# Kernel tuning notes

Measured on AMD Instinct MI355X. Metric: run time of the kernel, lower is better.

Reference implementation:

```python
import jax, jax.numpy as jnp
import numpy as np
from jax import lax

EPS = 1e-8

def int8_fq(x):
    # Int8ActPerTensorFloat: per-tensor float scale from runtime max-abs, fake-quant with STE.
    s = jnp.maximum(jnp.max(jnp.abs(x)) / 127.0, EPS)
    q = jnp.clip(jnp.round(x / s), -128.0, 127.0) * s
    return x + lax.stop_gradient(q - x)

def bin_w(w):
    # BINARY weight quant: per-tensor scale = mean(|w|), weights -> +/- scale (STE).
    s = jnp.mean(jnp.abs(w))
    wq = jnp.where(w >= 0, s, -s)
    return w + lax.stop_gradient(wq - w)

def qrelu(x):
    # QuantReLU with int8 input_quant and int8 act_quant
    return int8_fq(jax.nn.relu(int8_fq(x)))

def conv2d(x, w, b):
    y = lax.conv_general_dilated(x, w, window_strides=(1, 1), padding='VALID',
                                 dimension_numbers=('NCHW', 'OIHW', 'NCHW'))
    return y + b[None, :, None, None]

def maxpool2(x):
    return lax.reduce_window(x, -jnp.inf, lax.max, (1, 1, 2, 2), (1, 1, 2, 2), 'VALID')

def setup_inputs() -> dict:
    key = jax.random.key(0)
    ks = jax.random.split(key, 12)
    B = 16384
    inp = {
        'input_tensor': jax.random.normal(ks[0], (B, 3, 32, 32), dtype=jnp.float32),
        'w1': jax.random.normal(ks[1], (6, 3, 5, 5), dtype=jnp.float32) * 0.1,
        'b1': jax.random.normal(ks[2], (6,), dtype=jnp.float32) * 0.01,
        'w2': jax.random.normal(ks[3], (16, 6, 5, 5), dtype=jnp.float32) * 0.1,
        'b2': jax.random.normal(ks[4], (16,), dtype=jnp.float32) * 0.01,
        'fw1': jax.random.normal(ks[5], (120, 400), dtype=jnp.float32) * 0.05,
        'fb1': jax.random.normal(ks[6], (120,), dtype=jnp.float32) * 0.01,
        'fw2': jax.random.normal(ks[7], (84, 120), dtype=jnp.float32) * 0.05,
        'fb2': jax.random.normal(ks[8], (84,), dtype=jnp.float32) * 0.01,
        'fw3': jax.random.normal(ks[9], (10, 84), dtype=jnp.float32) * 0.05,
        'fb3': jax.random.normal(ks[10], (10,), dtype=jnp.float32) * 0.01,
    }
    return inp

def reference(input_tensor, w1, b1, w2, b2, fw1, fb1, fw2, fb2, fw3, fb3):
    x = int8_fq(input_tensor)                  # QuantIdentity
    x = qrelu(conv2d(x, bin_w(w1), b1))        # conv1 + relu1: [B,6,28,28]
    x = maxpool2(x)                            # [B,6,14,14]
    x = qrelu(conv2d(x, bin_w(w2), b2))        # conv2 + relu2: [B,16,10,10]
    x = maxpool2(x)                            # [B,16,5,5]
    x = x.reshape(x.shape[0], -1)              # [B,400]
    x = qrelu(x @ bin_w(fw1).T + fb1)          # fc1 + relu3: [B,120]
    x = qrelu(x @ bin_w(fw2).T + fb2)          # fc2 + relu4: [B,84]
    out = x @ bin_w(fw3).T + fb3               # fc3: [B,10]
    return out
```

## Files before the change

### kernel.cpp

```cpp
#include <hip/hip_runtime.h>
#include <math.h>

#define BATCH 16384
#define EPSQ 1e-8f

#define OFF_SCAL 0
#define OFF_WPK1 16
#define OFF_WPK2 196
#define OFF_FQ1  1156
#define OFF_FQ2  13156
#define OFF_FQ3  15844
#define OFF_A    16384
#define OFF_QIN   OFF_A
#define OFF_QC2   OFF_A
#define OFF_ISUM2 (OFF_A + 6000000)
#define OFF_QC3   (OFF_A + 10000000)
#define OFF_P3    (OFF_A + 12000000)
#define OFF_P4    (OFF_A + 14000000)
#define OFF_ISUM1 (OFF_A + 18874368)

__device__ inline int sdot4(unsigned int a, unsigned int b, int c) {
    return __builtin_amdgcn_sdot4((int)a, (int)b, c, false);
}

__device__ inline unsigned int fkey(float f) {
    unsigned int u = __float_as_uint(f);
    return (u & 0x80000000u) ? ~u : (u | 0x80000000u);
}
__device__ inline float fdec(unsigned int k) {
    unsigned int u = (k & 0x80000000u) ? (k ^ 0x80000000u) : ~k;
    return __uint_as_float(u);
}
#define KEY_ZERO   0x80000000u
#define KEY_NEGINF 0x007FFFFFu

__device__ inline float waveMax(float v) {
    #pragma unroll
    for (int off = 32; off > 0; off >>= 1)
        v = fmaxf(v, __shfl_down(v, off, 64));
    return v;
}

__device__ inline void blockAtomicMax2(float vmax, float vnmax,
                                       unsigned int* gmax, unsigned int* gnmax) {
    __shared__ float sm[4], sn[4];
    float a = waveMax(vmax), b = waveMax(vnmax);
    int tid = threadIdx.x;
    if ((tid & 63) == 0) { sm[tid >> 6] = a; sn[tid >> 6] = b; }
    __syncthreads();
    if (tid == 0) {
        atomicMax(gmax, fkey(fmaxf(fmaxf(sm[0], sm[1]), fmaxf(sm[2], sm[3]))));
        atomicMax(gnmax, fkey(fmaxf(fmaxf(sn[0], sn[1]), fmaxf(sn[2], sn[3]))));
    }
}

__device__ inline void block2AtomicMax2(float vmax, float vnmax,
                                        unsigned int* gmax, unsigned int* gnmax) {
    __shared__ float sm[2], sn[2];
    float a = waveMax(vmax), b = waveMax(vnmax);
    int tid = threadIdx.x;
    if ((tid & 63) == 0) { sm[tid >> 6] = a; sn[tid >> 6] = b; }
    __syncthreads();
    if (tid == 0) {
        atomicMax(gmax, fkey(fmaxf(sm[0], sm[1])));
        atomicMax(gnmax, fkey(fmaxf(sn[0], sn[1])));
    }
}

__device__ inline float fq_elem(float x, float s) {
    float q = fminf(fmaxf(rintf(x / s), -128.0f), 127.0f);
    return q * s;
}
__device__ inline int qrelu_code(float x, float s1, float s2) {
    float q = fq_elem(x, s1);
    q = fmaxf(q, 0.0f);
    return (int)fminf(fmaxf(rintf(q / s2), -128.0f), 127.0f);
}
__device__ inline void get_qrelu_scales(const unsigned int* scalu, int slot,
                                        float& s1, float& s2) {
    float maxa = fdec(scalu[slot]), negm = fdec(scalu[slot + 1]);
    float absm = fmaxf(maxa, negm);
    s1 = fmaxf(absm / 127.0f, EPSQ);
    float qm = fminf(fmaxf(rintf(maxa / s1), -128.0f), 127.0f) * s1;
    s2 = fmaxf(fmaxf(qm, 0.0f) / 127.0f, EPSQ);
}

__device__ inline unsigned int sgn8(float w) { return (w >= 0.0f) ? 0x01u : 0xFFu; }

__device__ inline unsigned int u32at(const unsigned int* wv, int wi, int k) {
    return (k == 0) ? wv[wi]
        : __builtin_amdgcn_perm(wv[wi + 1], wv[wi], 0x03020100u + 0x01010101u * (unsigned)k);
}

__global__ __launch_bounds__(256) void prep_kernel(const float* __restrict__ w1,
        const float* __restrict__ w2, const float* __restrict__ fw1,
        const float* __restrict__ fw2, const float* __restrict__ fw3,
        float* __restrict__ wsf) {
    int blk = blockIdx.x, tid = threadIdx.x;
    unsigned int* wsu = (unsigned int*)wsf;
    if (blk == 0) {
        if (tid == 0) wsu[0] = KEY_ZERO;
        else if (tid <= 8) wsu[tid] = KEY_NEGINF;
        return;
    }
    const float* src = nullptr; int N = 0;
    if (blk == 1)      { src = w1;  N = 450; }
    else if (blk == 2) { src = w2;  N = 2400; }
    else if (blk == 3) { src = fw1; N = 48000; }
    else if (blk == 4) { src = fw2; N = 10080; }
    else               { src = fw3; N = 840; }
    __shared__ float red[256];
    float partial = 0.0f;
    for (int i = tid; i < N; i += 256) partial += fabsf(src[i]);
    red[tid] = partial;
    __syncthreads();
    for (int s = 128; s > 0; s >>= 1) {
        if (tid < s) red[tid] += red[tid + s];
        __syncthreads();
    }
    if (tid == 0) wsf[8 + blk] = red[0] / (float)N;

    if (blk == 1) {
        for (int t = tid; t < 90; t += 256) {
            const float* wp = w1 + t * 5;
            wsu[OFF_WPK1 + 2*t] = sgn8(wp[0]) | (sgn8(wp[1])<<8) | (sgn8(wp[2])<<16) | (sgn8(wp[3])<<24);
            wsu[OFF_WPK1 + 2*t + 1] = sgn8(wp[4]) << 24;
        }
    } else if (blk == 2) {
        for (int t = tid; t < 480; t += 256) {
            const float* wp = w2 + t * 5;
            wsu[OFF_WPK2 + 2*t] = sgn8(wp[0]) | (sgn8(wp[1])<<8) | (sgn8(wp[2])<<16) | (sgn8(wp[3])<<24);
            wsu[OFF_WPK2 + 2*t + 1] = sgn8(wp[4]) << 24;
        }
    } else if (blk == 3) {
        for (int i = tid; i < 12000; i += 256) {
            int j = i / 100, k = i % 100;
            const float* wp = fw1 + j * 400 + k * 4;
            wsu[OFF_FQ1 + i] = sgn8(wp[0]) | (sgn8(wp[1])<<8) | (sgn8(wp[2])<<16) | (sgn8(wp[3])<<24);
        }
    } else if (blk == 4) {
        for (int i = tid; i < 2688; i += 256) {
            int j = i >> 5, k = i & 31;
            unsigned int u = 0;
            if (k < 30) {
                const float* wp = fw2 + j * 120 + k * 4;
                u = sgn8(wp[0]) | (sgn8(wp[1])<<8) | (sgn8(wp[2])<<16) | (sgn8(wp[3])<<24);
            }
            wsu[OFF_FQ2 + i] = u;
        }
    } else {
        for (int i = tid; i < 240; i += 256) {
            int j = i / 24, k = i % 24;
            unsigned int u = 0;
            if (k < 21) {
                const float* wp = fw3 + j * 84 + k * 4;
                u = sgn8(wp[0]) | (sgn8(wp[1])<<8) | (sgn8(wp[2])<<16) | (sgn8(wp[3])<<24);
            }
            wsu[OFF_FQ3 + i] = u;
        }
    }
}

__global__ __launch_bounds__(256) void absmax_kernel(const float4* __restrict__ x, int n4,
                                                     unsigned int* __restrict__ gkey) {
    float m = 0.0f;
    int stride = gridDim.x * 256;
    for (int i = blockIdx.x * 256 + threadIdx.x; i < n4; i += stride) {
        float4 v = x[i];
        m = fmaxf(m, fmaxf(fmaxf(fabsf(v.x), fabsf(v.y)), fmaxf(fabsf(v.z), fabsf(v.w))));
    }
    __shared__ float sm[4];
    m = waveMax(m);
    int tid = threadIdx.x;
    if ((tid & 63) == 0) sm[tid >> 6] = m;
    __syncthreads();
    if (tid == 0)
        atomicMax(gkey, fkey(fmaxf(fmaxf(sm[0], sm[1]), fmaxf(sm[2], sm[3]))));
}

__global__ __launch_bounds__(256) void quant1_kernel(const float4* __restrict__ x,
                                                     float* __restrict__ wsf) {
    unsigned int* wsu = (unsigned int*)wsf;
    float s0 = fmaxf(fdec(wsu[0]) / 127.0f, EPSQ);
    unsigned int* qin = wsu + OFF_QIN;
    int stride = gridDim.x * 256;
    const int total = BATCH * 96 * 12;
    for (int unit = blockIdx.x * 256 + threadIdx.x; unit < total; unit += stride) {
        int row_id = unit / 12, w = unit % 12;
        unsigned int u = 0;
        if (w < 8) {
            float4 v = x[row_id * 8 + w];
            int q0 = (int)fminf(fmaxf(rintf(v.x / s0), -128.f), 127.f);
            int q1 = (int)fminf(fmaxf(rintf(v.y / s0), -128.f), 127.f);
            int q2 = (int)fminf(fmaxf(rintf(v.z / s0), -128.f), 127.f);
            int q3 = (int)fminf(fmaxf(rintf(v.w / s0), -128.f), 127.f);
            u = (q0 & 255) | ((q1 & 255) << 8) | ((q2 & 255) << 16) | ((unsigned)(q3 & 255) << 24);
        }
        qin[unit] = u;
    }
}

#define C1_ROWP 48
#define C1_CIS  1536
#define C1_IMGS 4608

template<int PH>
__device__ __forceinline__ void c1_phase(const unsigned char* ib, const unsigned int* wcp,
                                         int* ip, int& gmax, int& gmin) {
    int a0[14], a1[14];
    #pragma unroll
    for (int i = 0; i < 14; i++) { a0[i] = 0; a1[i] = 0; }
    #pragma unroll 1
    for (int ci = 0; ci < 3; ci++) {
        uint4 A[6]; unsigned int Bv[6];
        const unsigned char* cb = ib + ci * C1_CIS;
        #pragma unroll
        for (int r = 0; r < 6; r++) {
            const unsigned char* rb = cb + r * C1_ROWP;
            if (PH == 0) {
                A[r]  = *(const uint4*)(rb);
                Bv[r] = *(const unsigned int*)(rb + 16);
            } else {
                Bv[r] = *(const unsigned int*)(rb + 12);
                A[r]  = *(const uint4*)(rb + 16);
            }
        }
        const unsigned int* wkp = wcp + ci * 10;
        unsigned int wk0[5], wk4[5];
        #pragma unroll
        for (int ky = 0; ky < 5; ky++) { wk0[ky] = wkp[2*ky]; wk4[ky] = wkp[2*ky+1]; }
        #pragma unroll
        for (int r6 = 0; r6 < 6; r6++) {
            unsigned int wq[5];
            if (PH == 0) {
                wq[0] = A[r6].x; wq[1] = A[r6].y; wq[2] = A[r6].z; wq[3] = A[r6].w; wq[4] = Bv[r6];
            } else {
                wq[0] = __builtin_amdgcn_perm(A[r6].x, Bv[r6],  0x05040302u);
                wq[1] = __builtin_amdgcn_perm(A[r6].y, A[r6].x, 0x05040302u);
                wq[2] = __builtin_amdgcn_perm(A[r6].z, A[r6].y, 0x05040302u);
                wq[3] = __builtin_amdgcn_perm(A[r6].w, A[r6].z, 0x05040302u);
                wq[4] = __builtin_amdgcn_perm(A[r6].w, A[r6].w, 0x00000302u);
            }
            unsigned int up[15];
            #pragma unroll
            for (int i = 0; i < 15; i++) up[i] = u32at(wq, i >> 2, i & 3);
            if (r6 <= 4) {
                unsigned int w0 = wk0[r6], w4 = wk4[r6];
                #pragma unroll
                for (int i = 0; i < 14; i++) {
                    a0[i] = sdot4(up[i], w0, a0[i]);
                    a0[i] = sdot4(up[i+1], w4, a0[i]);
                }
            }
            if (r6 >= 1) {
                unsigned int w0 = wk0[r6-1], w4 = wk4[r6-1];
                #pragma unroll
                for (int i = 0; i < 14; i++) {
                    a1[i] = sdot4(up[i], w0, a1[i]);
                    a1[i] = sdot4(up[i+1], w4, a1[i]);
                }
            }
        }
    }
    #pragma unroll
    for (int i = 0; i < 14; i++) {
        gmax = max(gmax, max(a0[i], a1[i]));
        gmin = min(gmin, min(a0[i], a1[i]));
    }
    #pragma unroll
    for (int p = 0; p < 7; p++)
        ip[p] = max(max(a0[2*p], a0[2*p+1]), max(a1[2*p], a1[2*p+1]));
}

__global__ __launch_bounds__(256) void conv1_kernel(const float* __restrict__ b1,
                                                    float* __restrict__ wsf) {
    __shared__ __align__(16) unsigned char xq[6 * C1_IMGS];
    __shared__ unsigned int wpk[180];
    __shared__ float bsm[6];
    unsigned int* wsu = (unsigned int*)wsf;
    int tid = threadIdx.x;
    int b0 = blockIdx.x * 6;
    int nimg = min(6, BATCH - b0);
    float s0 = fmaxf(fdec(wsu[0]) / 127.0f, EPSQ);
    float seff = s0 * wsf[9];

    {
        const uint4* src = (const uint4*)((const unsigned char*)(wsu + OFF_QIN) + (size_t)b0 * C1_IMGS);
        uint4* dst = (uint4*)xq;
        for (int i = tid; i < nimg * 288; i += 256) dst[i] = src[i];
    }
    for (int i = tid; i < 180; i += 256) wpk[i] = wsu[OFF_WPK1 + i];
    if (tid < 6) bsm[tid] = b1[tid];
    __syncthreads();

    unsigned int* isum1 = wsu + OFF_ISUM1;
    float vmax = -INFINITY, vnmax = -INFINITY;
    int ntask = nimg * 84;
    for (int t = tid; t < ntask; t += 256) {
        int img = t / 84, r = t % 84;
        int c = r / 14, py = r % 14;
        const unsigned char* ib = &xq[img * C1_IMGS + (2 * py) * C1_ROWP];
        const unsigned int* wcp = &wpk[c * 30];
        int ip0[7], ip1[7];
        int gmax = -2000000000, gmin = 2000000000;
        c1_phase<0>(ib, wcp, ip0, gmax, gmin);
        c1_phase<1>(ib, wcp, ip1, gmax, gmin);
        float bias = bsm[c];
        vmax  = fmaxf(vmax,  fmaf(seff, (float)gmax, bias));
        vnmax = fmaxf(vnmax, -fmaf(seff, (float)gmin, bias));
        unsigned int* dst = isum1 + 588 * (size_t)(b0 + img) + 7 * (c * 14 + py);
        #pragma unroll
        for (int p = 0; p < 7; p++) {
            int lo = (p < 7) ? ((p & 1) ? ip1[0] : 0) : 0; (void)lo;
        }
        int v14[14];
        #pragma unroll
        for (int p = 0; p < 7; p++) { v14[p] = ip0[p]; v14[7 + p] = ip1[p]; }
        #pragma unroll
        for (int p = 0; p < 7; p++)
            dst[p] = (v14[2*p] & 0xFFFF) | ((unsigned)(v14[2*p+1] & 0xFFFF) << 16);
    }
    blockAtomicMax2(vmax, vnmax, wsu + 1, wsu + 2);
}

__global__ __launch_bounds__(256) void quant2_kernel(const float* __restrict__ b1,
                                                     float* __restrict__ wsf) {
    unsigned int* wsu = (unsigned int*)wsf;
    float s1, s2;
    get_qrelu_scales(wsu, 1, s1, s2);
    float s0 = fmaxf(fdec(wsu[0]) / 127.0f, EPSQ);
    float seff = s0 * wsf[9];
    float bv[6];
    #pragma unroll
    for (int c = 0; c < 6; c++) bv[c] = b1[c];
    const short* isum1 = (const short*)(wsu + OFF_ISUM1);
    unsigned int* qc2 = wsu + OFF_QC2;
    int stride = gridDim.x * 256;
    const int total = BATCH * 84 * 4;
    for (int unit = blockIdx.x * 256 + threadIdx.x; unit < total; unit += stride) {
        int row_id = unit >> 2, w = unit & 3;
        int bci = row_id / 14, row = row_id % 14;
        int ci = bci % 6;
        float bias = bv[ci];
        unsigned int u = 0;
        const short* sp = isum1 + (size_t)bci * 196 + row * 14;
        #pragma unroll
        for (int k = 0; k < 4; k++) {
            int col = w * 4 + k;
            int code = 0;
            if (col < 14) {
                float pre = fmaf(seff, (float)sp[col], bias);
                code = qrelu_code(pre, s1, s2);
            }
            u |= ((unsigned)(code & 255)) << (8 * k);
        }
        qc2[unit] = u;
    }
}

#define C2_ROWP 16
#define C2_CIS  224
#define C2_IMGS 1344

__global__ __launch_bounds__(256) void conv2_kernel(const float* __restrict__ b2,
                                                    float* __restrict__ wsf) {
    __shared__ __align__(16) unsigned char act[6 * C2_IMGS];
    __shared__ unsigned int wpk[960];
    __shared__ float bsm[16];
    unsigned int* wsu = (unsigned int*)wsf;
    int tid = threadIdx.x;
    int b0 = blockIdx.x * 6;
    int nimg = min(6, BATCH - b0);
    float s1, s2;
    get_qrelu_scales(wsu, 1, s1, s2);
    float seff = s2 * wsf[10];

    {
        const uint4* src = (const uint4*)((const unsigned char*)(wsu + OFF_QC2) + (size_t)b0 * C2_IMGS);
        uint4* dst = (uint4*)act;
        for (int i = tid; i < nimg * 84; i += 256) dst[i] = src[i];
    }
    for (int i = tid; i < 960; i += 256) wpk[i] = wsu[OFF_WPK2 + i];
    if (tid < 16) bsm[tid] = b2[tid];
    __syncthreads();

    short* isum2 = (short*)(wsu + OFF_ISUM2);
    float vmax = -INFINITY, vnmax = -INFINITY;
    int ntask = nimg * 80;
    for (int t = tid; t < ntask; t += 256) {
        int img = t / 80, r = t % 80;
        int c = r / 5, py = r % 5;
        const unsigned char* ib = &act[img * C2_IMGS + (2 * py) * C2_ROWP];
        int a0[10], a1[10];
        #pragma unroll
        for (int i = 0; i < 10; i++) { a0[i] = 0; a1[i] = 0; }
        #pragma unroll 1
        for (int cig = 0; cig < 3; cig++) {
            uint4 R[2][6];
            #pragma unroll
            for (int g = 0; g < 2; g++)
                #pragma unroll
                for (int r6 = 0; r6 < 6; r6++)
                    R[g][r6] = *(const uint4*)(ib + (2*cig + g) * C2_CIS + r6 * C2_ROWP);
            #pragma unroll
            for (int g = 0; g < 2; g++) {
                int ci = 2*cig + g;
                const unsigned int* wkp = &wpk[(c * 6 + ci) * 10];
                unsigned int wk0[5], wk4[5];
                #pragma unroll
                for (int ky = 0; ky < 5; ky++) { wk0[ky] = wkp[2*ky]; wk4[ky] = wkp[2*ky+1]; }
                #pragma unroll
                for (int r6 = 0; r6 < 6; r6++) {
                    unsigned int wv[4] = { R[g][r6].x, R[g][r6].y, R[g][r6].z, R[g][r6].w };
                    unsigned int up[11];
                    #pragma unroll
                    for (int i = 0; i < 11; i++) up[i] = u32at(wv, i >> 2, i & 3);
                    if (r6 <= 4) {
                        unsigned int w0 = wk0[r6], w4 = wk4[r6];
                        #pragma unroll
                        for (int i = 0; i < 10; i++) {
                            a0[i] = sdot4(up[i], w0, a0[i]);
                            a0[i] = sdot4(up[i+1], w4, a0[i]);
                        }
                    }
                    if (r6 >= 1) {
                        unsigned int w0 = wk0[r6-1], w4 = wk4[r6-1];
                        #pragma unroll
                        for (int i = 0; i < 10; i++) {
                            a1[i] = sdot4(up[i], w0, a1[i]);
                            a1[i] = sdot4(up[i+1], w4, a1[i]);
                        }
                    }
                }
            }
        }
        int gmax = -2000000000, gmin = 2000000000;
        #pragma unroll
        for (int i = 0; i < 10; i++) {
            gmax = max(gmax, max(a0[i], a1[i]));
            gmin = min(gmin, min(a0[i], a1[i]));
        }
        float bias = bsm[c];
        vmax  = fmaxf(vmax,  fmaf(seff, (float)gmax, bias));
        vnmax = fmaxf(vnmax, -fmaf(seff, (float)gmin, bias));
        short* dst = isum2 + (size_t)(b0 + img) * 400 + c * 25 + py * 5;
        #pragma unroll
        for (int p = 0; p < 5; p++)
            dst[p] = (short)max(max(a0[2*p], a0[2*p+1]), max(a1[2*p], a1[2*p+1]));
    }
    blockAtomicMax2(vmax, vnmax, wsu + 3, wsu + 4);
}

__global__ __launch_bounds__(256) void quant3_kernel(const float* __restrict__ b2,
                                                     float* __restrict__ wsf) {
    unsigned int* wsu = (unsigned int*)wsf;
    float s1, s2;
    get_qrelu_scales(wsu, 3, s1, s2);
    float sp1, sp2;
    get_qrelu_scales(wsu, 1, sp1, sp2);
    float seff = sp2 * wsf[10];
    __shared__ float bv[16];
    if (threadIdx.x < 16) bv[threadIdx.x] = b2[threadIdx.x];
    __syncthreads();
    const short* isum2 = (const short*)(wsu + OFF_ISUM2);
    unsigned int* qc3 = wsu + OFF_QC3;
    int stride = gridDim.x * 256;
    const int total = BATCH * 100;
    for (int unit = blockIdx.x * 256 + threadIdx.x; unit < total; unit += stride) {
        int b = unit / 100, w = unit % 100;
        const short* sp = isum2 + (size_t)b * 400 + w * 4;
        unsigned int u = 0;
        #pragma unroll
        for (int k = 0; k < 4; k++) {
            int p = w * 4 + k;
            float pre = fmaf(seff, (float)sp[k], bv[p / 25]);
            int code = qrelu_code(pre, s1, s2);
            u |= ((unsigned)(code & 255)) << (8 * k);
        }
        qc3[unit] = u;
    }
}

__global__ __launch_bounds__(128) void fc1_kernel(const float* __restrict__ fb1,
                                                  float* __restrict__ wsf) {
    __shared__ unsigned int xs[8][100];
    __shared__ __align__(16) float pb[960];
    unsigned int* wsu = (unsigned int*)wsf;
    float* p3 = wsf + OFF_P3;
    int tid = threadIdx.x;
    size_t row0 = (size_t)blockIdx.x * 8;
    float s1, s2;
    get_qrelu_scales(wsu, 3, s1, s2);
    float seff = s2 * wsf[11];
    {
        const uint4* src = (const uint4*)(wsu + OFF_QC3 + row0 * 100);
        uint4* dst = (uint4*)xs;
        for (int i = tid; i < 200; i += 128) dst[i] = src[i];
    }
    __syncthreads();
    float vmax = -INFINITY, vnmax = -INFINITY;
    if (tid < 120) {
        int j = tid;
        int acc[8];
        #pragma unroll
        for (int r = 0; r < 8; r++) acc[r] = 0;
        const uint4* wrow = (const uint4*)&wsu[OFF_FQ1 + j * 100];
        for (int kg = 0; kg < 25; kg++) {
            uint4 wv = wrow[kg];
            #pragma unroll
            for (int r = 0; r < 8; r++) {
                uint4 xv = *(const uint4*)&xs[r][kg * 4];
                acc[r] = sdot4(xv.x, wv.x, acc[r]);
                acc[r] = sdot4(xv.y, wv.y, acc[r]);
                acc[r] = sdot4(xv.z, wv.z, acc[r]);
                acc[r] = sdot4(xv.w, wv.w, acc[r]);
            }
        }
        float bias = fb1[j];
        #pragma unroll
        for (int r = 0; r < 8; r++) {
            float pv = fmaf(seff, (float)acc[r], bias);
            pb[r * 120 + j] = pv;
            vmax = fmaxf(vmax, pv); vnmax = fmaxf(vnmax, -pv);
        }
    }
    __syncthreads();
    {
        const float4* pb4 = (const float4*)pb;
        float4* d4 = (float4*)(p3 + row0 * 120);
        for (int i = tid; i < 240; i += 128) d4[i] = pb4[i];
    }
    block2AtomicMax2(vmax, vnmax, wsu + 5, wsu + 6);
}

__global__ __launch_bounds__(128) void fc2_kernel(const float* __restrict__ fb2,
                                                  float* __restrict__ wsf) {
    __shared__ unsigned int xs[8][32];
    __shared__ __align__(16) float pb[672];
    unsigned int* wsu = (unsigned int*)wsf;
    const float* p3 = wsf + OFF_P3;
    float* p4 = wsf + OFF_P4;
    int tid = threadIdx.x;
    size_t row0 = (size_t)blockIdx.x * 8;
    float s1, s2;
    get_qrelu_scales(wsu, 5, s1, s2);
    float seff = s2 * wsf[12];
    const float4* src = (const float4*)(p3 + row0 * 120);
    for (int i = tid; i < 240; i += 128) {
        float4 v = src[i];
        int c0 = qrelu_code(v.x, s1, s2), c1 = qrelu_code(v.y, s1, s2);
        int c2 = qrelu_code(v.z, s1, s2), c3 = qrelu_code(v.w, s1, s2);
        xs[i / 30][i % 30] = c0 | (c1 << 8) | (c2 << 16) | ((unsigned)c3 << 24);
    }
    if (tid < 16) xs[tid >> 1][30 + (tid & 1)] = 0;
    __syncthreads();
    float vmax = -INFINITY, vnmax = -INFINITY;
    if (tid < 84) {
        int j = tid;
        int acc[8];
        #pragma unroll
        for (int r = 0; r < 8; r++) acc[r] = 0;
        const uint4* wrow = (const uint4*)&wsu[OFF_FQ2 + j * 32];
        #pragma unroll
        for (int kg = 0; kg < 8; kg++) {
            uint4 wv = wrow[kg];
            #pragma unroll
            for (int r = 0; r < 8; r++) {
                uint4 xv = *(const uint4*)&xs[r][kg * 4];
                acc[r] = sdot4(xv.x, wv.x, acc[r]);
                acc[r] = sdot4(xv.y, wv.y, acc[r]);
                acc[r] = sdot4(xv.z, wv.z, acc[r]);
                acc[r] = sdot4(xv.w, wv.w, acc[r]);
            }
        }
        float bias = fb2[j];
        #pragma unroll
        for (int r = 0; r < 8; r++) {
            float pv = fmaf(seff, (float)acc[r], bias);
            pb[r * 84 + j] = pv;
            vmax = fmaxf(vmax, pv); vnmax = fmaxf(vnmax, -pv);
        }
    }
    __syncthreads();
    {
        const float4* pb4 = (const float4*)pb;
        float4* d4 = (float4*)(p4 + row0 * 84);
        for (int i = tid; i < 168; i += 128) d4[i] = pb4[i];
    }
    block2AtomicMax2(vmax, vnmax, wsu + 7, wsu + 8);
}

__global__ __launch_bounds__(256) void fc3_kernel(const float* __restrict__ fb3,
                                                  float* __restrict__ out,
                                                  float* __restrict__ wsf) {
    __shared__ unsigned int wsm[240];
    __shared__ float bs[10];
    __shared__ __align__(16) float pb[2560];
    unsigned int* wsu = (unsigned int*)wsf;
    const float* p4 = wsf + OFF_P4;
    int tid = threadIdx.x;
    for (int i = tid; i < 240; i += 256) wsm[i] = wsu[OFF_FQ3 + i];
    if (tid < 10) bs[tid] = fb3[tid];
    __syncthreads();
    float s1, s2;
    get_qrelu_scales(wsu, 7, s1, s2);
    float seff = s2 * wsf[13];
    size_t row = (size_t)blockIdx.x * 256 + tid;
    unsigned int xr[24];
    const float4* src = (const float4*)(p4 + row * 84);
    #pragma unroll
    for (int k = 0; k < 21; k++) {
        float4 v = src[k];
        int c0 = qrelu_code(v.x, s1, s2), c1 = qrelu_code(v.y, s1, s2);
        int c2 = qrelu_code(v.z, s1, s2), c3 = qrelu_code(v.w, s1, s2);
        xr[k] = c0 | (c1 << 8) | (c2 << 16) | ((unsigned)c3 << 24);
    }
    xr[21] = 0; xr[22] = 0; xr[23] = 0;
    #pragma unroll
    for (int j = 0; j < 10; j++) {
        int acc = 0;
        #pragma unroll
        for (int k = 0; k < 24; k++) acc = sdot4(xr[k], wsm[j * 24 + k], acc);
        pb[tid * 10 + j] = fmaf(seff, (float)acc, bs[j]);
    }
    __syncthreads();
    {
        const float4* pb4 = (const float4*)pb;
        float4* d4 = (float4*)(out + (size_t)blockIdx.x * 2560);
        for (int i = tid; i < 640; i += 256) d4[i] = pb4[i];
    }
}

extern "C" void kernel_launch(void* const* d_in, const int* in_sizes, int n_in,
                              void* d_out, int out_size, void* d_ws, size_t ws_size,
                              hipStream_t stream) {
    const float* input = (const float*)d_in[0];
    const float* w1  = (const float*)d_in[1];
    const float* b1  = (const float*)d_in[2];
    const float* w2  = (const float*)d_in[3];
    const float* b2  = (const float*)d_in[4];
    const float* fw1 = (const float*)d_in[5];
    const float* fb1 = (const float*)d_in[6];
    const float* fw2 = (const float*)d_in[7];
    const float* fb2 = (const float*)d_in[8];
    const float* fw3 = (const float*)d_in[9];
    const float* fb3 = (const float*)d_in[10];
    float* ws  = (float*)d_ws;
    float* out = (float*)d_out;

    prep_kernel<<<6, 256, 0, stream>>>(w1, w2, fw1, fw2, fw3, ws);
    absmax_kernel<<<2048, 256, 0, stream>>>((const float4*)input,
                                            (int)((size_t)BATCH * 3072 / 4),
                                            (unsigned int*)ws);
    quant1_kernel<<<8192, 256, 0, stream>>>((const float4*)input, ws);
    conv1_kernel<<<(BATCH + 5) / 6, 256, 0, stream>>>(b1, ws);
    quant2_kernel<<<4096, 256, 0, stream>>>(b1, ws);
    conv2_kernel<<<(BATCH + 5) / 6, 256, 0, stream>>>(b2, ws);
    quant3_kernel<<<2048, 256, 0, stream>>>(b2, ws);
    fc1_kernel<<<BATCH / 8, 128, 0, stream>>>(fb1, ws);
    fc2_kernel<<<BATCH / 8, 128, 0, stream>>>(fb2, ws);
    fc3_kernel<<<BATCH / 256, 256, 0, stream>>>(fb3, out, ws);
}
```

Baseline: 581.8 us.

## Interleave even/odd rows in conv inputs and widen FC blocks to 256 threads

The quant kernels now store activation rows in even/odd-interleaved order, so each pooled output row's six source rows sit in a compact slot pattern, and conv1/conv2 index rows through that permutation. conv2's per-channel stride is padded from 224 to 256 bytes, which enlarges the QC2 buffer and pushes the ISUM2 offset up. fc1 and fc2 now process 16 and 24 rows per 256-thread block instead of 8 rows per 128 threads, improving occupancy and amortising the weight loads. fc2 gains a tail guard because 16384 is not divisible by 24. The layout change mainly targets LDS bank conflicts in the conv inner loops and adds padding traffic in exchange.

New measurement: 524.4 us. 1.11x faster.

```diff
diff --git a/kernel.cpp b/kernel.cpp
--- a/kernel.cpp
+++ b/kernel.cpp
@@ -13,7 +13,7 @@
 #define OFF_A    16384
 #define OFF_QIN   OFF_A
 #define OFF_QC2   OFF_A
-#define OFF_ISUM2 (OFF_A + 6000000)
+#define OFF_ISUM2 (OFF_A + 6400000)
 #define OFF_QC3   (OFF_A + 10000000)
 #define OFF_P3    (OFF_A + 12000000)
 #define OFF_P4    (OFF_A + 14000000)
@@ -51,19 +51,6 @@
     if (tid == 0) {
         atomicMax(gmax, fkey(fmaxf(fmaxf(sm[0], sm[1]), fmaxf(sm[2], sm[3]))));
         atomicMax(gnmax, fkey(fmaxf(fmaxf(sn[0], sn[1]), fmaxf(sn[2], sn[3]))));
-    }
-}
-
-__device__ inline void block2AtomicMax2(float vmax, float vnmax,
-                                        unsigned int* gmax, unsigned int* gnmax) {
-    __shared__ float sm[2], sn[2];
-    float a = waveMax(vmax), b = waveMax(vnmax);
-    int tid = threadIdx.x;
-    if ((tid & 63) == 0) { sm[tid >> 6] = a; sn[tid >> 6] = b; }
-    __syncthreads();
-    if (tid == 0) {
-        atomicMax(gmax, fkey(fmaxf(sm[0], sm[1])));
-        atomicMax(gnmax, fkey(fmaxf(sn[0], sn[1])));
     }
 }
 
@@ -187,6 +174,8 @@
     const int total = BATCH * 96 * 12;
     for (int unit = blockIdx.x * 256 + threadIdx.x; unit < total; unit += stride) {
         int row_id = unit / 12, w = unit % 12;
+        int plane = row_id >> 5, row = row_id & 31;
+        int slot = (row >> 1) + ((row & 1) << 4);
         unsigned int u = 0;
         if (w < 8) {
             float4 v = x[row_id * 8 + w];
@@ -196,7 +185,7 @@
             int q3 = (int)fminf(fmaxf(rintf(v.w / s0), -128.f), 127.f);
             u = (q0 & 255) | ((q1 & 255) << 8) | ((q2 & 255) << 16) | ((unsigned)(q3 & 255) << 24);
         }
-        qin[unit] = u;
+        qin[(plane * 32 + slot) * 12 + w] = u;
     }
 }
 
@@ -216,7 +205,7 @@
         const unsigned char* cb = ib + ci * C1_CIS;
         #pragma unroll
         for (int r = 0; r < 6; r++) {
-            const unsigned char* rb = cb + r * C1_ROWP;
+            const unsigned char* rb = cb + (((r & 1) << 4) + (r >> 1)) * C1_ROWP;
             if (PH == 0) {
                 A[r]  = *(const uint4*)(rb);
                 Bv[r] = *(const unsigned int*)(rb + 16);
@@ -299,7 +288,7 @@
     for (int t = tid; t < ntask; t += 256) {
         int img = t / 84, r = t % 84;
         int c = r / 14, py = r % 14;
-        const unsigned char* ib = &xq[img * C1_IMGS + (2 * py) * C1_ROWP];
+        const unsigned char* ib = &xq[img * C1_IMGS + py * C1_ROWP];
         const unsigned int* wcp = &wpk[c * 30];
         int ip0[7], ip1[7];
         int gmax = -2000000000, gmin = 2000000000;
@@ -309,10 +298,6 @@
         vmax  = fmaxf(vmax,  fmaf(seff, (float)gmax, bias));
         vnmax = fmaxf(vnmax, -fmaf(seff, (float)gmin, bias));
         unsigned int* dst = isum1 + 588 * (size_t)(b0 + img) + 7 * (c * 14 + py);
-        #pragma unroll
-        for (int p = 0; p < 7; p++) {
-            int lo = (p < 7) ? ((p & 1) ? ip1[0] : 0) : 0; (void)lo;
-        }
         int v14[14];
         #pragma unroll
         for (int p = 0; p < 7; p++) { v14[p] = ip0[p]; v14[7 + p] = ip1[p]; }
@@ -341,6 +326,7 @@
         int row_id = unit >> 2, w = unit & 3;
         int bci = row_id / 14, row = row_id % 14;
         int ci = bci % 6;
+        int slot = (row >> 1) + ((row & 1) << 3);
         float bias = bv[ci];
         unsigned int u = 0;
         const short* sp = isum1 + (size_t)bci * 196 + row * 14;
@@ -354,13 +340,13 @@
             }
             u |= ((unsigned)(code & 255)) << (8 * k);
         }
-        qc2[unit] = u;
+        qc2[((size_t)bci * 16 + slot) * 4 + w] = u;
     }
 }
 
 #define C2_ROWP 16
-#define C2_CIS  224
-#define C2_IMGS 1344
+#define C2_CIS  256
+#define C2_IMGS 1536
 
 __global__ __launch_bounds__(256) void conv2_kernel(const float* __restrict__ b2,
                                                     float* __restrict__ wsf) {
@@ -378,7 +364,7 @@
     {
         const uint4* src = (const uint4*)((const unsigned char*)(wsu + OFF_QC2) + (size_t)b0 * C2_IMGS);
         uint4* dst = (uint4*)act;
-        for (int i = tid; i < nimg * 84; i += 256) dst[i] = src[i];
+        for (int i = tid; i < nimg * 96; i += 256) dst[i] = src[i];
     }
     for (int i = tid; i < 960; i += 256) wpk[i] = wsu[OFF_WPK2 + i];
     if (tid < 16) bsm[tid] = b2[tid];
@@ -390,7 +376,7 @@
     for (int t = tid; t < ntask; t += 256) {
         int img = t / 80, r = t % 80;
         int c = r / 5, py = r % 5;
-        const unsigned char* ib = &act[img * C2_IMGS + (2 * py) * C2_ROWP];
+        const unsigned char* ib = &act[img * C2_IMGS + py * C2_ROWP];
         int a0[10], a1[10];
         #pragma unroll
         for (int i = 0; i < 10; i++) { a0[i] = 0; a1[i] = 0; }
@@ -401,7 +387,8 @@
             for (int g = 0; g < 2; g++)
                 #pragma unroll
                 for (int r6 = 0; r6 < 6; r6++)
-                    R[g][r6] = *(const uint4*)(ib + (2*cig + g) * C2_CIS + r6 * C2_ROWP);
+                    R[g][r6] = *(const uint4*)(ib + (2*cig + g) * C2_CIS
+                                + (((r6 & 1) << 3) + (r6 >> 1)) * C2_ROWP);
             #pragma unroll
             for (int g = 0; g < 2; g++) {
                 int ci = 2*cig + g;
@@ -481,26 +468,26 @@
     }
 }
 
-__global__ __launch_bounds__(128) void fc1_kernel(const float* __restrict__ fb1,
+__global__ __launch_bounds__(256) void fc1_kernel(const float* __restrict__ fb1,
                                                   float* __restrict__ wsf) {
-    __shared__ unsigned int xs[8][100];
-    __shared__ __align__(16) float pb[960];
+    __shared__ unsigned int xs[16][100];
+    __shared__ __align__(16) float pb[1920];
     unsigned int* wsu = (unsigned int*)wsf;
     float* p3 = wsf + OFF_P3;
     int tid = threadIdx.x;
-    size_t row0 = (size_t)blockIdx.x * 8;
+    size_t row0 = (size_t)blockIdx.x * 16;
     float s1, s2;
     get_qrelu_scales(wsu, 3, s1, s2);
     float seff = s2 * wsf[11];
     {
         const uint4* src = (const uint4*)(wsu + OFF_QC3 + row0 * 100);
         uint4* dst = (uint4*)xs;
-        for (int i = tid; i < 200; i += 128) dst[i] = src[i];
+        for (int i = tid; i < 400; i += 256) dst[i] = src[i];
     }
     __syncthreads();
     float vmax = -INFINITY, vnmax = -INFINITY;
-    if (tid < 120) {
-        int j = tid;
+    if (tid < 240) {
+        int g = tid / 120, j = tid % 120;
         int acc[8];
         #pragma unroll
         for (int r = 0; r < 8; r++) acc[r] = 0;
@@ -509,7 +496,7 @@
             uint4 wv = wrow[kg];
             #pragma unroll
             for (int r = 0; r < 8; r++) {
-                uint4 xv = *(const uint4*)&xs[r][kg * 4];
+                uint4 xv = *(const uint4*)&xs[g * 8 + r][kg * 4];
                 acc[r] = sdot4(xv.x, wv.x, acc[r]);
                 acc[r] = sdot4(xv.y, wv.y, acc[r]);
                 acc[r] = sdot4(xv.z, wv.z, acc[r]);
@@ -520,7 +507,7 @@
         #pragma unroll
         for (int r = 0; r < 8; r++) {
             float pv = fmaf(seff, (float)acc[r], bias);
-            pb[r * 120 + j] = pv;
+            pb[(g * 8 + r) * 120 + j] = pv;
             vmax = fmaxf(vmax, pv); vnmax = fmaxf(vnmax, -pv);
         }
     }
@@ -528,35 +515,36 @@
     {
         const float4* pb4 = (const float4*)pb;
         float4* d4 = (float4*)(p3 + row0 * 120);
-        for (int i = tid; i < 240; i += 128) d4[i] = pb4[i];
-    }
-    block2AtomicMax2(vmax, vnmax, wsu + 5, wsu + 6);
-}
-
-__global__ __launch_bounds__(128) void fc2_kernel(const float* __restrict__ fb2,
+        for (int i = tid; i < 480; i += 256) d4[i] = pb4[i];
+    }
+    blockAtomicMax2(vmax, vnmax, wsu + 5, wsu + 6);
+}
+
+__global__ __launch_bounds__(256) void fc2_kernel(const float* __restrict__ fb2,
                                                   float* __restrict__ wsf) {
-    __shared__ unsigned int xs[8][32];
-    __shared__ __align__(16) float pb[672];
+    __shared__ unsigned int xs[24][32];
+    __shared__ __align__(16) float pb[2016];
     unsigned int* wsu = (unsigned int*)wsf;
     const float* p3 = wsf + OFF_P3;
     float* p4 = wsf + OFF_P4;
     int tid = threadIdx.x;
-    size_t row0 = (size_t)blockIdx.x * 8;
+    size_t row0 = (size_t)blockIdx.x * 24;
+    int nrow = min(24, (int)(BATCH - row0));
     float s1, s2;
     get_qrelu_scales(wsu, 5, s1, s2);
     float seff = s2 * wsf[12];
     const float4* src = (const float4*)(p3 + row0 * 120);
-    for (int i = tid; i < 240; i += 128) {
+    for (int i = tid; i < nrow * 30; i += 256) {
         float4 v = src[i];
         int c0 = qrelu_code(v.x, s1, s2), c1 = qrelu_code(v.y, s1, s2);
         int c2 = qrelu_code(v.z, s1, s2), c3 = qrelu_code(v.w, s1, s2);
         xs[i / 30][i % 30] = c0 | (c1 << 8) | (c2 << 16) | ((unsigned)c3 << 24);
     }
-    if (tid < 16) xs[tid >> 1][30 + (tid & 1)] = 0;
+    if (tid < 24) { xs[tid][30] = 0; xs[tid][31] = 0; }
     __syncthreads();
     float vmax = -INFINITY, vnmax = -INFINITY;
-    if (tid < 84) {
-        int j = tid;
+    if (tid < 252) {
+        int g = tid / 84, j = tid % 84;
         int acc[8];
         #pragma unroll
         for (int r = 0; r < 8; r++) acc[r] = 0;
@@ -566,7 +554,7 @@
             uint4 wv = wrow[kg];
             #pragma unroll
             for (int r = 0; r < 8; r++) {
-                uint4 xv = *(const uint4*)&xs[r][kg * 4];
+                uint4 xv = *(const uint4*)&xs[g * 8 + r][kg * 4];
                 acc[r] = sdot4(xv.x, wv.x, acc[r]);
                 acc[r] = sdot4(xv.y, wv.y, acc[r]);
                 acc[r] = sdot4(xv.z, wv.z, acc[r]);
@@ -576,18 +564,21 @@
         float bias = fb2[j];
         #pragma unroll
         for (int r = 0; r < 8; r++) {
-            float pv = fmaf(seff, (float)acc[r], bias);
-            pb[r * 84 + j] = pv;
-            vmax = fmaxf(vmax, pv); vnmax = fmaxf(vnmax, -pv);
+            int lr = g * 8 + r;
+            if (lr < nrow) {
+                float pv = fmaf(seff, (float)acc[r], bias);
+                pb[lr * 84 + j] = pv;
+                vmax = fmaxf(vmax, pv); vnmax = fmaxf(vnmax, -pv);
+            }
         }
     }
     __syncthreads();
     {
         const float4* pb4 = (const float4*)pb;
         float4* d4 = (float4*)(p4 + row0 * 84);
-        for (int i = tid; i < 168; i += 128) d4[i] = pb4[i];
-    }
-    block2AtomicMax2(vmax, vnmax, wsu + 7, wsu + 8);
+        for (int i = tid; i < nrow * 21; i += 256) d4[i] = pb4[i];
+    }
+    blockAtomicMax2(vmax, vnmax, wsu + 7, wsu + 8);
 }
 
 __global__ __launch_bounds__(256) void fc3_kernel(const float* __restrict__ fb3,
@@ -657,7 +648,7 @@
     quant2_kernel<<<4096, 256, 0, stream>>>(b1, ws);
     conv2_kernel<<<(BATCH + 5) / 6, 256, 0, stream>>>(b2, ws);
     quant3_kernel<<<2048, 256, 0, stream>>>(b2, ws);
-    fc1_kernel<<<BATCH / 8, 128, 0, stream>>>(fb1, ws);
-    fc2_kernel<<<BATCH / 8, 128, 0, stream>>>(fb2, ws);
+    fc1_kernel<<<BATCH / 16, 256, 0, stream>>>(fb1, ws);
+    fc2_kernel<<<(BATCH + 23) / 24, 256, 0, stream>>>(fb2, ws);
     fc3_kernel<<<BATCH / 256, 256, 0, stream>>>(fb3, out, ws);
 }
```
